# Performance work log

Hardware: AMD Instinct MI355X
Metric: run time of the kernel (lower is better)

Reference implementation:

```python
import jax, jax.numpy as jnp
import numpy as np

B = 4; D = 256; H = 8; L = 4; P = 4; DFF = 1024; DH = D // H
SHAPES = ((64, 64), (32, 32), (16, 16), (8, 8))
LEN = sum(h * w for h, w in SHAPES)  # 5440


def setup_inputs() -> dict:
    key = jax.random.key(0)
    ks = jax.random.split(key, 12)
    s = 0.02
    ss = jnp.array(SHAPES, jnp.int32)
    lsi = jnp.array(np.concatenate([[0], np.cumsum([h * w for h, w in SHAPES])[:-1]]), jnp.int32)
    return dict(
        src=jax.random.normal(ks[0], (B, LEN, D), jnp.float32),
        reference_points=jax.random.uniform(ks[1], (B, LEN, L, 2), jnp.float32),
        spatial_shapes=ss,
        level_start_index=lsi,
        padding_mask=jnp.zeros((B, LEN), bool),
        pos=jax.random.normal(ks[2], (B, LEN, D), jnp.float32),
        W_value=s * jax.random.normal(ks[3], (D, D), jnp.float32), b_value=jnp.zeros(D, jnp.float32),
        W_off=s * jax.random.normal(ks[4], (D, H * L * P * 2), jnp.float32), b_off=jnp.zeros(H * L * P * 2, jnp.float32),
        W_attn=s * jax.random.normal(ks[5], (D, H * L * P), jnp.float32), b_attn=jnp.zeros(H * L * P, jnp.float32),
        W_out=s * jax.random.normal(ks[6], (D, D), jnp.float32), b_out=jnp.zeros(D, jnp.float32),
        ln1_g=jnp.ones(D, jnp.float32), ln1_b=jnp.zeros(D, jnp.float32),
        W1=s * jax.random.normal(ks[7], (D, DFF), jnp.float32), b1=jnp.zeros(DFF, jnp.float32),
        W2=s * jax.random.normal(ks[8], (DFF, D), jnp.float32), b2=jnp.zeros(D, jnp.float32),
        ln2_g=jnp.ones(D, jnp.float32), ln2_b=jnp.zeros(D, jnp.float32),
    )


def layer_norm(x, g, b, eps=1e-5):
    m = jnp.mean(x, -1, keepdims=True)
    v = jnp.var(x, -1, keepdims=True)
    return (x - m) * jax.lax.rsqrt(v + eps) * g + b


def ms_deform_attn(query, src, reference_points, spatial_shapes, level_start_index, padding_mask,
                   W_value, b_value, W_off, b_off, W_attn, b_attn, W_out, b_out):
    Bq, Lq, C = query.shape
    Lin = src.shape[1]
    value = src @ W_value + b_value
    value = jnp.where(padding_mask[..., None], jnp.zeros((), value.dtype), value)
    value = value.reshape(Bq, Lin, H, DH).transpose(0, 2, 1, 3)  # [B,H,Lin,d]

    off = (query @ W_off + b_off).reshape(Bq, Lq, H, L, P, 2)
    attn = (query @ W_attn + b_attn).reshape(Bq, Lq, H, L * P)
    attn = jax.nn.softmax(attn, axis=-1).reshape(Bq, Lq, H, L, P)

    # offset normalizer is (W_l, H_l)
    norm = jnp.stack([spatial_shapes[:, 1], spatial_shapes[:, 0]], -1).astype(query.dtype)  # [L,2]
    loc = reference_points[:, :, None, :, None, :] + off / norm[None, None, None, :, None, :]  # [B,Lq,H,L,P,2]

    Hl = spatial_shapes[:, 0][None, None, None, :, None]  # [1,1,1,L,1]
    Wl = spatial_shapes[:, 1][None, None, None, :, None]
    start = level_start_index[None, None, None, :, None]
    # grid_sample align_corners=False: pixel = loc * size - 0.5
    px = loc[..., 0] * Wl.astype(query.dtype) - 0.5  # [B,Lq,H,L,P]
    py = loc[..., 1] * Hl.astype(query.dtype) - 0.5
    x0 = jnp.floor(px); y0 = jnp.floor(py)
    fx = px - x0; fy = py - y0
    x0i = x0.astype(jnp.int32); y0i = y0.astype(jnp.int32)

    out = jnp.zeros((Bq, Lq, H, DH), query.dtype)
    corners = ((0, 0, (1 - fx) * (1 - fy)), (1, 0, fx * (1 - fy)), (0, 1, (1 - fx) * fy), (1, 1, fx * fy))
    for dx, dy, cw in corners:
        xi = x0i + dx
        yi = y0i + dy
        valid = (xi >= 0) & (xi < Wl) & (yi >= 0) & (yi < Hl)  # zeros padding
        flat = start + jnp.clip(yi, 0, Hl - 1) * Wl + jnp.clip(xi, 0, Wl - 1)  # [B,Lq,H,L,P]
        w = attn * cw * valid.astype(query.dtype)  # [B,Lq,H,L,P]
        idx = flat.transpose(0, 2, 1, 3, 4).reshape(Bq, H, Lq * L * P)  # [B,H,N]
        g = jnp.take_along_axis(value, idx[..., None], axis=2)  # [B,H,N,d]
        g = g.reshape(Bq, H, Lq, L, P, DH)
        out = out + jnp.einsum('bqhlp,bhqlpd->bqhd', w, g)

    out = out.reshape(Bq, Lq, C)
    return out @ W_out + b_out


def reference(src, reference_points, spatial_shapes, level_start_index, padding_mask, pos,
              W_value, b_value, W_off, b_off, W_attn, b_attn, W_out, b_out,
              ln1_g, ln1_b, W1, b1, W2, b2, ln2_g, ln2_b):
    q = src + pos
    src2 = ms_deform_attn(q, src, reference_points, spatial_shapes, level_start_index, padding_mask,
                          W_value, b_value, W_off, b_off, W_attn, b_attn, W_out, b_out)
    x = layer_norm(src + src2, ln1_g, ln1_b)  # dropout is identity at eval
    ff = jax.nn.relu(x @ W1 + b1) @ W2 + b2
    return layer_norm(x + ff, ln2_g, ln2_b)
```

## Files before the change

### kernel.cpp

```cpp
#include <hip/hip_runtime.h>
#include <hip/hip_fp16.h>

constexpr int NB   = 4;
constexpr int SLEN = 5440;
constexpr long NTOK = (long)NB * SLEN;
constexpr int DD   = 256;
constexpr int NH   = 8;
constexpr int DHD  = 32;
constexpr int NL   = 4;
constexpr int NP   = 4;
constexpr int DFF  = 1024;

typedef __attribute__((ext_vector_type(8))) short short8;
typedef __attribute__((ext_vector_type(8))) unsigned short ushort8;
typedef __attribute__((ext_vector_type(4))) float f32x4;

static __device__ __forceinline__ unsigned short f2bf(float x) {
  union { float f; unsigned int u; } v; v.f = x;
  unsigned int r = v.u + 0x7fffu + ((v.u >> 16) & 1u);
  return (unsigned short)(r >> 16);
}
static __device__ __forceinline__ float bf2f(unsigned short u) {
  union { unsigned int i; float f; } v; v.i = ((unsigned int)u) << 16; return v.f;
}
static __device__ __forceinline__ unsigned int pack2bf(float lo, float hi) {
  return (unsigned int)f2bf(lo) | ((unsigned int)f2bf(hi) << 16);
}
static __device__ __forceinline__ unsigned int pack2h_dup(float a) {
  const unsigned int h = (unsigned int)__half_as_ushort(__float2half(a));
  return h | (h << 16);
}
static __device__ __forceinline__ __half2 u2h2(unsigned int u) {
  union { unsigned int i; __half2 h; } c; c.i = u; return c.h;
}

static __device__ __forceinline__ long fragpos(int k, int n, int KT) {
  const int kt = k >> 5, i = k & 7;
  const int lane = ((k >> 3) & 3) * 16 + (n & 15);
  const int nt = n >> 4;
  return (((long)(nt * KT + kt) * 64 + lane) * 8 + i);
}

__global__ __launch_bounds__(256) void k_prep_all(const float* __restrict__ W1,
                                                  const float* __restrict__ W2,
                                                  const float* __restrict__ Wv,
                                                  const float* __restrict__ Woff,
                                                  const float* __restrict__ Wattn,
                                                  const float* __restrict__ Wo,
                                                  unsigned short* __restrict__ W1f,
                                                  unsigned short* __restrict__ W2f,
                                                  unsigned short* __restrict__ Wvf,
                                                  unsigned short* __restrict__ Wqf,
                                                  unsigned short* __restrict__ Wof) {
  const int g = blockIdx.x * 256 + threadIdx.x;
  if (g < 262144) {
    const int k = g >> 10, n = g & 1023;
    W1f[fragpos(k, n, 8)] = f2bf(W1[g]);
  } else if (g < 524288) {
    const int g2 = g - 262144;
    const int k = g2 >> 8, n = g2 & 255;
    W2f[fragpos(k, n, 32)] = f2bf(W2[g2]);
  } else if (g < 589824) {
    const int g2 = g - 524288;
    const int k = g2 >> 8, n = g2 & 255;
    Wvf[fragpos(k, n, 8)] = f2bf(Wv[g2]);
  } else if (g < 688128) {
    const int g2 = g - 589824;
    const int k = g2 / 384, n = g2 % 384;
    const float w = (n < 256) ? Woff[k * 256 + n] : Wattn[k * 128 + (n - 256)];
    Wqf[fragpos(k, n, 8)] = f2bf(w);
  } else if (g < 753664) {
    const int g2 = g - 688128;
    const int k = g2 >> 8, n = g2 & 255;
    Wof[fragpos(k, n, 8)] = f2bf(Wo[g2]);
  }
}

__global__ __launch_bounds__(256) void k_vq2(const float* __restrict__ src,
                                             const float* __restrict__ pos,
                                             const unsigned short* __restrict__ Wvf,
                                             const float* __restrict__ bv,
                                             const unsigned short* __restrict__ Wqf,
                                             const float* __restrict__ boff,
                                             const float* __restrict__ battn,
                                             unsigned short* __restrict__ valh,
                                             unsigned short* __restrict__ offbf,
                                             float* __restrict__ attn) {
  __shared__ unsigned short Xs[32 * 256];
  const int t = threadIdx.x;
  const int w = t >> 6, lane = t & 63;
  const int lr = lane & 15, lgrp = lane >> 4;
  const long row0 = (long)blockIdx.x * 32;
  const int r = t >> 3;
  const int c0 = (t & 7) * 32;

  {
    const float* sp = &src[(row0 + r) * DD + c0];
#pragma unroll
    for (int j = 0; j < 4; ++j) {
      const float4 a = *reinterpret_cast<const float4*>(&sp[j * 8 + 0]);
      const float4 b = *reinterpret_cast<const float4*>(&sp[j * 8 + 4]);
      short8 pk;
      pk[0] = (short)f2bf(a.x); pk[1] = (short)f2bf(a.y);
      pk[2] = (short)f2bf(a.z); pk[3] = (short)f2bf(a.w);
      pk[4] = (short)f2bf(b.x); pk[5] = (short)f2bf(b.y);
      pk[6] = (short)f2bf(b.z); pk[7] = (short)f2bf(b.w);
      int byte = r * 512 + (c0 + j * 8) * 2;
      byte ^= (r & 7) << 4;
      *reinterpret_cast<short8*>(reinterpret_cast<char*>(Xs) + byte) = pk;
    }
  }
  __syncthreads();

  short8 af[2][8];
#pragma unroll
  for (int mt = 0; mt < 2; ++mt)
#pragma unroll
    for (int kt = 0; kt < 8; ++kt) {
      const int row = mt * 16 + lr;
      int byte = row * 512 + kt * 64 + lgrp * 16;
      byte ^= (row & 7) << 4;
      af[mt][kt] = *reinterpret_cast<const short8*>(reinterpret_cast<const char*>(Xs) + byte);
    }

  {
    f32x4 acc[2][4];
#pragma unroll
    for (int mt = 0; mt < 2; ++mt)
#pragma unroll
      for (int n = 0; n < 4; ++n) acc[mt][n] = (f32x4){0.f, 0.f, 0.f, 0.f};
#pragma unroll
    for (int n = 0; n < 4; ++n) {
      const int nt = w * 4 + n;
#pragma unroll
      for (int kt = 0; kt < 8; ++kt) {
        const short8 bf_ = *reinterpret_cast<const short8*>(&Wvf[((nt * 8 + kt) * 64 + lane) * 8]);
#pragma unroll
        for (int mt = 0; mt < 2; ++mt)
          acc[mt][n] = __builtin_amdgcn_mfma_f32_16x16x32_bf16(af[mt][kt], bf_, acc[mt][n], 0, 0, 0);
      }
    }
#pragma unroll
    for (int n = 0; n < 4; ++n) {
      const int col = w * 64 + n * 16 + lr;
      const float bb = bv[col];
#pragma unroll
      for (int mt = 0; mt < 2; ++mt)
#pragma unroll
        for (int j = 0; j < 4; ++j) {
          const int row = mt * 16 + lgrp * 4 + j;
          valh[(row0 + row) * DD + col] =
              __half_as_ushort(__float2half(acc[mt][n][j] + bb));
        }
    }
  }
  __syncthreads();

  {
    const float* pp = &pos[(row0 + r) * DD + c0];
#pragma unroll
    for (int j = 0; j < 4; ++j) {
      const float4 c = *reinterpret_cast<const float4*>(&pp[j * 8 + 0]);
      const float4 d = *reinterpret_cast<const float4*>(&pp[j * 8 + 4]);
      int byte = r * 512 + (c0 + j * 8) * 2;
      byte ^= (r & 7) << 4;
      short8 pk = *reinterpret_cast<const short8*>(reinterpret_cast<const char*>(Xs) + byte);
      pk[0] = (short)f2bf(bf2f((unsigned short)pk[0]) + c.x);
      pk[1] = (short)f2bf(bf2f((unsigned short)pk[1]) + c.y);
      pk[2] = (short)f2bf(bf2f((unsigned short)pk[2]) + c.z);
      pk[3] = (short)f2bf(bf2f((unsigned short)pk[3]) + c.w);
      pk[4] = (short)f2bf(bf2f((unsigned short)pk[4]) + d.x);
      pk[5] = (short)f2bf(bf2f((unsigned short)pk[5]) + d.y);
      pk[6] = (short)f2bf(bf2f((unsigned short)pk[6]) + d.z);
      pk[7] = (short)f2bf(bf2f((unsigned short)pk[7]) + d.w);
      *reinterpret_cast<short8*>(reinterpret_cast<char*>(Xs) + byte) = pk;
    }
  }
  __syncthreads();

#pragma unroll
  for (int mt = 0; mt < 2; ++mt)
#pragma unroll
    for (int kt = 0; kt < 8; ++kt) {
      const int row = mt * 16 + lr;
      int byte = row * 512 + kt * 64 + lgrp * 16;
      byte ^= (row & 7) << 4;
      af[mt][kt] = *reinterpret_cast<const short8*>(reinterpret_cast<const char*>(Xs) + byte);
    }

  {
    f32x4 acc[2][6];
#pragma unroll
    for (int mt = 0; mt < 2; ++mt)
#pragma unroll
      for (int i = 0; i < 6; ++i) acc[mt][i] = (f32x4){0.f, 0.f, 0.f, 0.f};
#pragma unroll
    for (int i = 0; i < 6; ++i) {
      const int ntg = w * 6 + i;
#pragma unroll
      for (int kt = 0; kt < 8; ++kt) {
        const short8 bf_ = *reinterpret_cast<const short8*>(&Wqf[((ntg * 8 + kt) * 64 + lane) * 8]);
#pragma unroll
        for (int mt = 0; mt < 2; ++mt)
          acc[mt][i] = __builtin_amdgcn_mfma_f32_16x16x32_bf16(af[mt][kt], bf_, acc[mt][i], 0, 0, 0);
      }
    }
#pragma unroll
    for (int i = 0; i < 6; ++i) {
      const int ntg = w * 6 + i;
      if (ntg < 16) {
        const int col = ntg * 16 + lr;
        const float bb = boff[col];
#pragma unroll
        for (int mt = 0; mt < 2; ++mt)
#pragma unroll
          for (int j = 0; j < 4; ++j) {
            const int row = mt * 16 + lgrp * 4 + j;
            offbf[(row0 + row) * 256 + col] = f2bf(acc[mt][i][j] + bb);
          }
      } else {
        const int na = ntg - 16;
        const float bb = battn[na * 16 + lr];
#pragma unroll
        for (int mt = 0; mt < 2; ++mt)
#pragma unroll
          for (int j = 0; j < 4; ++j) {
            const int row = mt * 16 + lgrp * 4 + j;
            const float v = acc[mt][i][j] + bb;
            float m = v;
#pragma unroll
            for (int d_ = 1; d_ <= 8; d_ <<= 1) m = fmaxf(m, __shfl_xor(m, d_, 16));
            const float e = __expf(v - m);
            float s = e;
#pragma unroll
            for (int d_ = 1; d_ <= 8; d_ <<= 1) s += __shfl_xor(s, d_, 16);
            attn[(row0 + row) * 128 + na * 16 + lr] = e / s;
          }
      }
    }
  }
}

__global__ __launch_bounds__(256) void k_sample6(const unsigned short* __restrict__ valh,
                                                 const unsigned short* __restrict__ offbf,
                                                 const float* __restrict__ attn,
                                                 const float* __restrict__ refp,
                                                 unsigned short* __restrict__ src2bf) {
  __shared__ int4  sIdx[4][2][8][16];
  __shared__ uint4 sWgt[4][2][8][16];
  const int t = threadIdx.x;
  const int w = t >> 6, lane = t & 63;
  const int tok = lane >> 5, hg = (lane >> 2) & 7, li = lane & 3;
  const int B = blockIdx.x;
  const int bimg = (B & 7) >> 1;
  const int ii = ((B >> 3) << 1) + (B & 1);
  const long n = (long)bimg * SLEN + ii * 8 + w * 2 + tok;
  const long bOff = (long)bimg * SLEN;

  const int   WlA[4] = {64, 32, 16, 8};
  const float rWA[4] = {1.f / 64.f, 1.f / 32.f, 1.f / 16.f, 1.f / 8.f};
  const int   stA[4] = {0, 4096, 5120, 5376};

#pragma unroll
  for (int q = 0; q < 4; ++q) {
    const int pt = q * 4 + li;
    const int Wi = WlA[q];
    const float Wf = (float)Wi, rW = rWA[q];
    const float rx = refp[(n * 4 + q) * 2 + 0];
    const float ry = refp[(n * 4 + q) * 2 + 1];
    const float aw = attn[n * 128 + hg * 16 + pt];
    const int oi = ((hg * 4 + q) * 4 + li) * 2;
    const unsigned int opk = *reinterpret_cast<const unsigned int*>(&offbf[n * 256 + oi]);
    const float ox = bf2f((unsigned short)(opk & 0xffff));
    const float oy = bf2f((unsigned short)(opk >> 16));
    const float px = (rx + ox * rW) * Wf - 0.5f;
    const float py = (ry + oy * rW) * Wf - 0.5f;
    const float x0f = floorf(px), y0f = floorf(py);
    const float fx = px - x0f, fy = py - y0f;
    const int x0 = (int)x0f, y0 = (int)y0f;
    int   ic[4];
    float wc[4];
#pragma unroll
    for (int c = 0; c < 4; ++c) {
      const int dx = c & 1, dy = c >> 1;
      const int xi = x0 + dx, yi = y0 + dy;
      const float cw = (dx ? fx : 1.f - fx) * (dy ? fy : 1.f - fy);
      const bool valid = (xi >= 0) && (xi < Wi) && (yi >= 0) && (yi < Wi);
      const int xc = min(max(xi, 0), Wi - 1);
      const int yc = min(max(yi, 0), Wi - 1);
      const long flat = stA[q] + yc * Wi + xc;
      ic[c] = (int)((bOff + flat) * DD + hg * DHD);
      wc[c] = aw * cw * (valid ? 1.f : 0.f);
    }
    const int slot = pt ^ hg;
    sIdx[w][tok][hg][slot] = make_int4(ic[0], ic[1], ic[2], ic[3]);
    sWgt[w][tok][hg][slot] = make_uint4(pack2h_dup(wc[0]), pack2h_dup(wc[1]),
                                        pack2h_dup(wc[2]), pack2h_dup(wc[3]));
  }
  __syncthreads();

  __half2 acc[4];
#pragma unroll
  for (int d = 0; d < 4; ++d) acc[d] = __float2half2_rn(0.f);
#pragma unroll 4
  for (int pt = 0; pt < 16; ++pt) {
    const int slot = pt ^ hg;
    const int4  ia = sIdx[w][tok][hg][slot];
    const uint4 wp = sWgt[w][tok][hg][slot];
    const uint4 u0 = *reinterpret_cast<const uint4*>(&valh[(long)ia.x + li * 8]);
    const uint4 u1 = *reinterpret_cast<const uint4*>(&valh[(long)ia.y + li * 8]);
    const uint4 u2 = *reinterpret_cast<const uint4*>(&valh[(long)ia.z + li * 8]);
    const uint4 u3 = *reinterpret_cast<const uint4*>(&valh[(long)ia.w + li * 8]);
    const __half2 w0 = u2h2(wp.x), w1 = u2h2(wp.y), w2 = u2h2(wp.z), w3 = u2h2(wp.w);
    acc[0] = __hfma2(u2h2(u0.x), w0, acc[0]);
    acc[1] = __hfma2(u2h2(u0.y), w0, acc[1]);
    acc[2] = __hfma2(u2h2(u0.z), w0, acc[2]);
    acc[3] = __hfma2(u2h2(u0.w), w0, acc[3]);
    acc[0] = __hfma2(u2h2(u1.x), w1, acc[0]);
    acc[1] = __hfma2(u2h2(u1.y), w1, acc[1]);
    acc[2] = __hfma2(u2h2(u1.z), w1, acc[2]);
    acc[3] = __hfma2(u2h2(u1.w), w1, acc[3]);
    acc[0] = __hfma2(u2h2(u2.x), w2, acc[0]);
    acc[1] = __hfma2(u2h2(u2.y), w2, acc[1]);
    acc[2] = __hfma2(u2h2(u2.z), w2, acc[2]);
    acc[3] = __hfma2(u2h2(u2.w), w2, acc[3]);
    acc[0] = __hfma2(u2h2(u3.x), w3, acc[0]);
    acc[1] = __hfma2(u2h2(u3.y), w3, acc[1]);
    acc[2] = __hfma2(u2h2(u3.z), w3, acc[2]);
    acc[3] = __hfma2(u2h2(u3.w), w3, acc[3]);
  }
  ushort8 o;
#pragma unroll
  for (int d = 0; d < 4; ++d) {
    o[2 * d]     = f2bf(__half2float(__low2half(acc[d])));
    o[2 * d + 1] = f2bf(__half2float(__high2half(acc[d])));
  }
  *reinterpret_cast<ushort8*>(&src2bf[n * DD + hg * DHD + li * 8]) = o;
}

__global__ __launch_bounds__(256) void k_outproj_mfma(const unsigned short* __restrict__ src2bf,
                                                      const unsigned short* __restrict__ Wof,
                                                      const float* __restrict__ bo,
                                                      const float* __restrict__ src,
                                                      const float* __restrict__ g1,
                                                      const float* __restrict__ b1g,
                                                      unsigned short* __restrict__ xbf) {
  __shared__ float rsum[32][4];
  __shared__ float rssq[32][4];
  const int t = threadIdx.x;
  const int w = t >> 6, lane = t & 63;
  const int lr = lane & 15, lgrp = lane >> 4;
  const long row0 = (long)blockIdx.x * 32;

  short8 af[2][8];
#pragma unroll
  for (int mt = 0; mt < 2; ++mt)
#pragma unroll
    for (int kt = 0; kt < 8; ++kt)
      af[mt][kt] = *reinterpret_cast<const short8*>(
          &src2bf[(row0 + mt * 16 + lr) * DD + kt * 32 + lgrp * 8]);

  f32x4 acc[2][4];
#pragma unroll
  for (int mt = 0; mt < 2; ++mt)
#pragma unroll
    for (int n = 0; n < 4; ++n) acc[mt][n] = (f32x4){0.f, 0.f, 0.f, 0.f};
#pragma unroll
  for (int n = 0; n < 4; ++n) {
    const int nt = w * 4 + n;
#pragma unroll
    for (int kt = 0; kt < 8; ++kt) {
      const short8 bf_ = *reinterpret_cast<const short8*>(&Wof[((nt * 8 + kt) * 64 + lane) * 8]);
#pragma unroll
      for (int mt = 0; mt < 2; ++mt)
        acc[mt][n] = __builtin_amdgcn_mfma_f32_16x16x32_bf16(af[mt][kt], bf_, acc[mt][n], 0, 0, 0);
    }
  }
  float bc[4], gc[4], bgc[4];
#pragma unroll
  for (int n = 0; n < 4; ++n) {
    const int col = w * 64 + n * 16 + lr;
    bc[n] = bo[col]; gc[n] = g1[col]; bgc[n] = b1g[col];
  }
  float vals[2][4][4];
#pragma unroll
  for (int mt = 0; mt < 2; ++mt)
#pragma unroll
    for (int j = 0; j < 4; ++j) {
      const int row = mt * 16 + lgrp * 4 + j;
      float s = 0.f, ss = 0.f;
#pragma unroll
      for (int n = 0; n < 4; ++n) {
        const int col = w * 64 + n * 16 + lr;
        const float v = acc[mt][n][j] + bc[n] + src[(row0 + row) * DD + col];
        vals[mt][n][j] = v;
        s += v; ss += v * v;
      }
#pragma unroll
      for (int m = 1; m <= 8; m <<= 1) { s += __shfl_xor(s, m, 64); ss += __shfl_xor(ss, m, 64); }
      if (lr == 0) { rsum[row][w] = s; rssq[row][w] = ss; }
    }
  __syncthreads();
#pragma unroll
  for (int mt = 0; mt < 2; ++mt)
#pragma unroll
    for (int j = 0; j < 4; ++j) {
      const int row = mt * 16 + lgrp * 4 + j;
      const float s  = rsum[row][0] + rsum[row][1] + rsum[row][2] + rsum[row][3];
      const float ss = rssq[row][0] + rssq[row][1] + rssq[row][2] + rssq[row][3];
      const float mean = s * (1.f / 256.f);
      const float inv  = rsqrtf(ss * (1.f / 256.f) - mean * mean + 1e-5f);
#pragma unroll
      for (int n = 0; n < 4; ++n) {
        const int col = w * 64 + n * 16 + lr;
        xbf[(row0 + row) * DD + col] = f2bf((vals[mt][n][j] - mean) * inv * gc[n] + bgc[n]);
      }
    }
}

__global__ __launch_bounds__(256) void k_ffn1e(const unsigned short* __restrict__ xbf,
                                               const unsigned short* __restrict__ W1f,
                                               const float* __restrict__ b1v,
                                               unsigned short* __restrict__ hfrag) {
  const int t = threadIdx.x;
  const int w = t >> 6, lane = t & 63;
  const int lr = lane & 15, lgrp = lane >> 4;
  const long row0 = (long)blockIdx.x * 64;
  const int hg = blockIdx.y;

  f32x4 acc[4][4];
#pragma unroll
  for (int mm = 0; mm < 4; ++mm)
#pragma unroll
    for (int n = 0; n < 4; ++n) acc[mm][n] = (f32x4){0.f, 0.f, 0.f, 0.f};

#pragma unroll
  for (int kt = 0; kt < 8; ++kt) {
    short8 bx[4];
#pragma unroll
    for (int n = 0; n < 4; ++n)
      bx[n] = *reinterpret_cast<const short8*>(
          &xbf[(row0 + n * 16 + lr) * DD + kt * 32 + lgrp * 8]);
#pragma unroll
    for (int mm = 0; mm < 4; ++mm) {
      const int ntg = hg * 16 + w * 4 + mm;
      const short8 aw1 = *reinterpret_cast<const short8*>(&W1f[((ntg * 8 + kt) * 64 + lane) * 8]);
#pragma unroll
      for (int n = 0; n < 4; ++n)
        acc[mm][n] = __builtin_amdgcn_mfma_f32_16x16x32_bf16(aw1, bx[n], acc[mm][n], 0, 0, 0);
    }
  }

#pragma unroll
  for (int mm = 0; mm < 4; ++mm) {
    const int ht = hg * 16 + w * 4 + mm;
    const float4 bq = *reinterpret_cast<const float4*>(&b1v[ht * 16 + lgrp * 4]);
#pragma unroll
    for (int n = 0; n < 4; ++n) {
      const long tt = (long)blockIdx.x * 4 + n;
      const long tbase = (tt * 64 + ht) * 256;
      int2 pk;
      pk.x = (int)pack2bf(fmaxf(acc[mm][n][0] + bq.x, 0.f),
                          fmaxf(acc[mm][n][1] + bq.y, 0.f));
      pk.y = (int)pack2bf(fmaxf(acc[mm][n][2] + bq.z, 0.f),
                          fmaxf(acc[mm][n][3] + bq.w, 0.f));
      *reinterpret_cast<int2*>(&hfrag[tbase + lane * 4]) = pk;
    }
  }
}

__global__ __launch_bounds__(256) void k_ffn2t(const unsigned short* __restrict__ hfrag,
                                               const unsigned short* __restrict__ W2f,
                                               const float* __restrict__ b2v_,
                                               const unsigned short* __restrict__ xbf,
                                               const float* __restrict__ g2,
                                               const float* __restrict__ b2g,
                                               float* __restrict__ outp) {
  __shared__ float rsum[32][4];
  __shared__ float rssq[32][4];
  const int t = threadIdx.x;
  const int w = t >> 6, lane = t & 63;
  const int lr = lane & 15, lgrp = lane >> 4;
  const long row0 = (long)blockIdx.x * 32;

  f32x4 acc[2][4];
#pragma unroll
  for (int mt = 0; mt < 2; ++mt)
#pragma unroll
    for (int n = 0; n < 4; ++n) acc[mt][n] = (f32x4){0.f, 0.f, 0.f, 0.f};

#pragma unroll 4
  for (int kt = 0; kt < 32; ++kt) {
    short8 ha[2];
#pragma unroll
    for (int mt = 0; mt < 2; ++mt) {
      const long tt = (row0 >> 4) + mt;
      const long tb = (tt * 64 + kt * 2 + (lgrp >> 1)) * 256;
      const unsigned short* tp = &hfrag[tb + (lgrp & 1) * 128 + lr * 4];
      union { short8 s8; struct { int2 lo, hi; } p; } u;
      u.p.lo = *reinterpret_cast<const int2*>(tp);
      u.p.hi = *reinterpret_cast<const int2*>(tp + 64);
      ha[mt] = u.s8;
    }
#pragma unroll
    for (int n = 0; n < 4; ++n) {
      const int nt = w * 4 + n;
      const short8 bf_ = *reinterpret_cast<const short8*>(&W2f[((nt * 32 + kt) * 64 + lane) * 8]);
#pragma unroll
      for (int mt = 0; mt < 2; ++mt)
        acc[mt][n] = __builtin_amdgcn_mfma_f32_16x16x32_bf16(ha[mt], bf_, acc[mt][n], 0, 0, 0);
    }
  }

  float b2c[4], g2c[4], bgc[4];
#pragma unroll
  for (int n = 0; n < 4; ++n) {
    const int col = w * 64 + n * 16 + lr;
    b2c[n] = b2v_[col]; g2c[n] = g2[col]; bgc[n] = b2g[col];
  }
  float vals[2][4][4];
#pragma unroll
  for (int mt = 0; mt < 2; ++mt)
#pragma unroll
    for (int j = 0; j < 4; ++j) {
      const int row = mt * 16 + lgrp * 4 + j;
      float s = 0.f, ss = 0.f;
#pragma unroll
      for (int n = 0; n < 4; ++n) {
        const int col = w * 64 + n * 16 + lr;
        const float v = acc[mt][n][j] + b2c[n] + bf2f(xbf[(row0 + row) * DD + col]);
        vals[mt][n][j] = v;
        s += v; ss += v * v;
      }
#pragma unroll
      for (int m = 1; m <= 8; m <<= 1) { s += __shfl_xor(s, m, 64); ss += __shfl_xor(ss, m, 64); }
      if (lr == 0) { rsum[row][w] = s; rssq[row][w] = ss; }
    }
  __syncthreads();
#pragma unroll
  for (int mt = 0; mt < 2; ++mt)
#pragma unroll
    for (int j = 0; j < 4; ++j) {
      const int row = mt * 16 + lgrp * 4 + j;
      const float s  = rsum[row][0] + rsum[row][1] + rsum[row][2] + rsum[row][3];
      const float ss = rssq[row][0] + rssq[row][1] + rssq[row][2] + rssq[row][3];
      const float mean = s * (1.f / 256.f);
      const float inv  = rsqrtf(ss * (1.f / 256.f) - mean * mean + 1e-5f);
#pragma unroll
      for (int n = 0; n < 4; ++n) {
        const int col = w * 64 + n * 16 + lr;
        outp[(row0 + row) * DD + col] = (vals[mt][n][j] - mean) * inv * g2c[n] + bgc[n];
      }
    }
}

extern "C" void kernel_launch(void* const* d_in, const int* in_sizes, int n_in,
                              void* d_out, int out_size, void* d_ws, size_t ws_size,
                              hipStream_t stream) {
  const float* src  = (const float*)d_in[0];
  const float* refp = (const float*)d_in[1];
  const float* pos  = (const float*)d_in[5];
  const float* Wv   = (const float*)d_in[6];
  const float* bv   = (const float*)d_in[7];
  const float* Woff = (const float*)d_in[8];
  const float* boff = (const float*)d_in[9];
  const float* Wat  = (const float*)d_in[10];
  const float* bat  = (const float*)d_in[11];
  const float* Wo   = (const float*)d_in[12];
  const float* bo   = (const float*)d_in[13];
  const float* g1   = (const float*)d_in[14];
  const float* b1g  = (const float*)d_in[15];
  const float* W1   = (const float*)d_in[16];
  const float* b1f  = (const float*)d_in[17];
  const float* W2   = (const float*)d_in[18];
  const float* b2f  = (const float*)d_in[19];
  const float* g2   = (const float*)d_in[20];
  const float* b2g  = (const float*)d_in[21];
  float* out = (float*)d_out;

  unsigned short* valh   = (unsigned short*)d_ws;
  unsigned short* offbf  = valh + NTOK * 256;
  float*          attn   = (float*)(offbf + NTOK * 256);
  unsigned short* src2bf = (unsigned short*)(attn + NTOK * 128);
  unsigned short* xbf    = src2bf + NTOK * 256;
  unsigned short* W1f = xbf + NTOK * 256;
  unsigned short* W2f = W1f + 262144;
  unsigned short* Wvf = W2f + 262144;
  unsigned short* Wqf = Wvf + 65536;
  unsigned short* Wof = Wqf + 98304;
  unsigned short* frag_end = Wof + 65536;
  const size_t used  = (size_t)((char*)frag_end - (char*)d_ws);
  const size_t hneed = (size_t)NTOK * 1024 * 2;
  unsigned short* hfrag = (used + hneed <= ws_size) ? frag_end
                                                    : (unsigned short*)d_ws;

  hipLaunchKernelGGL(k_prep_all, dim3(2944), dim3(256), 0, stream,
                     W1, W2, Wv, Woff, Wat, Wo, W1f, W2f, Wvf, Wqf, Wof);
  hipLaunchKernelGGL(k_vq2, dim3((int)(NTOK / 32)), dim3(256), 0, stream,
                     src, pos, Wvf, bv, Wqf, boff, bat, valh, offbf, attn);
  hipLaunchKernelGGL(k_sample6, dim3((int)(NTOK / 8)), dim3(256), 0, stream,
                     valh, offbf, attn, refp, src2bf);
  hipLaunchKernelGGL(k_outproj_mfma, dim3((int)(NTOK / 32)), dim3(256), 0, stream,
                     src2bf, Wof, bo, src, g1, b1g, xbf);
  hipLaunchKernelGGL(k_ffn1e, dim3((int)(NTOK / 64), 4), dim3(256), 0, stream,
                     xbf, W1f, b1f, hfrag);
  hipLaunchKernelGGL(k_ffn2t, dim3((int)(NTOK / 32)), dim3(256), 0, stream,
                     hfrag, W2f, b2f, xbf, g2, b2g, out);
}
```

Before: 160.0 us.

## Fuse out-projection, LayerNorm, FFN1 and FFN2 into one LDS-resident tail kernel

Merges the out-projection+LN1, FFN first layer and FFN second layer+LN2 kernels into a single kernel per 32-token block. The normalized activations and the 1024-wide hidden layer live in XOR-swizzled shared memory (80 KB) instead of round-tripping through global memory. This removes two launches and the global write and read of the hidden activations. The costs are lower occupancy from the large LDS allocation and W1 being re-read per 32-row block instead of per 64-row block.

```diff
diff --git a/kernel.cpp b/kernel.cpp
--- a/kernel.cpp
+++ b/kernel.cpp
@@ -338,15 +338,25 @@
   *reinterpret_cast<ushort8*>(&src2bf[n * DD + hg * DHD + li * 8]) = o;
 }
 
-__global__ __launch_bounds__(256) void k_outproj_mfma(const unsigned short* __restrict__ src2bf,
-                                                      const unsigned short* __restrict__ Wof,
-                                                      const float* __restrict__ bo,
-                                                      const float* __restrict__ src,
-                                                      const float* __restrict__ g1,
-                                                      const float* __restrict__ b1g,
-                                                      unsigned short* __restrict__ xbf) {
-  __shared__ float rsum[32][4];
-  __shared__ float rssq[32][4];
+__global__ __launch_bounds__(256) void k_tail(const unsigned short* __restrict__ src2bf,
+                                              const unsigned short* __restrict__ Wof,
+                                              const float* __restrict__ bo,
+                                              const float* __restrict__ src,
+                                              const float* __restrict__ g1,
+                                              const float* __restrict__ b1g,
+                                              const unsigned short* __restrict__ W1f,
+                                              const float* __restrict__ b1v,
+                                              const unsigned short* __restrict__ W2f,
+                                              const float* __restrict__ b2v_,
+                                              const float* __restrict__ g2,
+                                              const float* __restrict__ b2g,
+                                              float* __restrict__ outp) {
+  __shared__ char smem[81920];
+  unsigned short* Xls = (unsigned short*)smem;
+  unsigned short* Hls = (unsigned short*)(smem + 16384);
+  float* rsum = (float*)(smem + 16384);
+  float* rssq = rsum + 128;
+
   const int t = threadIdx.x;
   const int w = t >> 6, lane = t & 63;
   const int lr = lane & 15, lgrp = lane >> 4;
@@ -376,13 +386,132 @@
         acc[mt][n] = __builtin_amdgcn_mfma_f32_16x16x32_bf16(af[mt][kt], bf_, acc[mt][n], 0, 0, 0);
     }
   }
-  float bc[4], gc[4], bgc[4];
+  {
+    float bc[4], gc[4], bgc[4];
+#pragma unroll
+    for (int n = 0; n < 4; ++n) {
+      const int col = w * 64 + n * 16 + lr;
+      bc[n] = bo[col]; gc[n] = g1[col]; bgc[n] = b1g[col];
+    }
+    float vals[2][4][4];
+#pragma unroll
+    for (int mt = 0; mt < 2; ++mt)
+#pragma unroll
+      for (int j = 0; j < 4; ++j) {
+        const int row = mt * 16 + lgrp * 4 + j;
+        float s = 0.f, ss = 0.f;
+#pragma unroll
+        for (int n = 0; n < 4; ++n) {
+          const int col = w * 64 + n * 16 + lr;
+          const float v = acc[mt][n][j] + bc[n] + src[(row0 + row) * DD + col];
+          vals[mt][n][j] = v;
+          s += v; ss += v * v;
+        }
+#pragma unroll
+        for (int m = 1; m <= 8; m <<= 1) { s += __shfl_xor(s, m, 64); ss += __shfl_xor(ss, m, 64); }
+        if (lr == 0) { rsum[row * 4 + w] = s; rssq[row * 4 + w] = ss; }
+      }
+    __syncthreads();
+#pragma unroll
+    for (int mt = 0; mt < 2; ++mt)
+#pragma unroll
+      for (int j = 0; j < 4; ++j) {
+        const int row = mt * 16 + lgrp * 4 + j;
+        const float s  = rsum[row * 4 + 0] + rsum[row * 4 + 1] + rsum[row * 4 + 2] + rsum[row * 4 + 3];
+        const float ss = rssq[row * 4 + 0] + rssq[row * 4 + 1] + rssq[row * 4 + 2] + rssq[row * 4 + 3];
+        const float mean = s * (1.f / 256.f);
+        const float inv  = rsqrtf(ss * (1.f / 256.f) - mean * mean + 1e-5f);
+#pragma unroll
+        for (int n = 0; n < 4; ++n) {
+          const int col = w * 64 + n * 16 + lr;
+          const float xv = (vals[mt][n][j] - mean) * inv * gc[n] + bgc[n];
+          int byte = row * 512 + col * 2;
+          byte ^= (row & 7) << 4;
+          *reinterpret_cast<unsigned short*>(reinterpret_cast<char*>(Xls) + byte) = f2bf(xv);
+        }
+      }
+  }
+  __syncthreads();
+
+#pragma unroll
+  for (int hp = 0; hp < 2; ++hp) {
+    f32x4 a2[8][2];
+#pragma unroll
+    for (int mm = 0; mm < 8; ++mm)
+#pragma unroll
+      for (int n = 0; n < 2; ++n) a2[mm][n] = (f32x4){0.f, 0.f, 0.f, 0.f};
+#pragma unroll
+    for (int kt = 0; kt < 8; ++kt) {
+      short8 bx[2];
+#pragma unroll
+      for (int n = 0; n < 2; ++n) {
+        const int row = n * 16 + lr;
+        int byte = row * 512 + kt * 64 + lgrp * 16;
+        byte ^= (row & 7) << 4;
+        bx[n] = *reinterpret_cast<const short8*>(reinterpret_cast<const char*>(Xls) + byte);
+      }
+#pragma unroll
+      for (int mm = 0; mm < 8; ++mm) {
+        const int ntg = w * 16 + hp * 8 + mm;
+        const short8 aw1 = *reinterpret_cast<const short8*>(&W1f[((ntg * 8 + kt) * 64 + lane) * 8]);
+#pragma unroll
+        for (int n = 0; n < 2; ++n)
+          a2[mm][n] = __builtin_amdgcn_mfma_f32_16x16x32_bf16(aw1, bx[n], a2[mm][n], 0, 0, 0);
+      }
+    }
+#pragma unroll
+    for (int mm = 0; mm < 8; ++mm) {
+      const int ht = w * 16 + hp * 8 + mm;
+      const float4 bq = *reinterpret_cast<const float4*>(&b1v[ht * 16 + lgrp * 4]);
+#pragma unroll
+      for (int n = 0; n < 2; ++n) {
+        const int tok = n * 16 + lr;
+        int2 pk;
+        pk.x = (int)pack2bf(fmaxf(a2[mm][n][0] + bq.x, 0.f),
+                            fmaxf(a2[mm][n][1] + bq.y, 0.f));
+        pk.y = (int)pack2bf(fmaxf(a2[mm][n][2] + bq.z, 0.f),
+                            fmaxf(a2[mm][n][3] + bq.w, 0.f));
+        int byte = tok * 2048 + (ht * 16 + lgrp * 4) * 2;
+        byte ^= (tok & 7) << 4;
+        *reinterpret_cast<int2*>(reinterpret_cast<char*>(Hls) + byte) = pk;
+      }
+    }
+  }
+  __syncthreads();
+
+  f32x4 c2[2][4];
+#pragma unroll
+  for (int mt = 0; mt < 2; ++mt)
+#pragma unroll
+    for (int n = 0; n < 4; ++n) c2[mt][n] = (f32x4){0.f, 0.f, 0.f, 0.f};
+#pragma unroll 4
+  for (int kt = 0; kt < 32; ++kt) {
+    short8 ha[2];
+#pragma unroll
+    for (int mt = 0; mt < 2; ++mt) {
+      const int row = mt * 16 + lr;
+      int byte = row * 2048 + kt * 64 + lgrp * 16;
+      byte ^= (row & 7) << 4;
+      ha[mt] = *reinterpret_cast<const short8*>(reinterpret_cast<const char*>(Hls) + byte);
+    }
+#pragma unroll
+    for (int n = 0; n < 4; ++n) {
+      const int nt = w * 4 + n;
+      const short8 bf_ = *reinterpret_cast<const short8*>(&W2f[((nt * 32 + kt) * 64 + lane) * 8]);
+#pragma unroll
+      for (int mt = 0; mt < 2; ++mt)
+        c2[mt][n] = __builtin_amdgcn_mfma_f32_16x16x32_bf16(ha[mt], bf_, c2[mt][n], 0, 0, 0);
+    }
+  }
+
+  float b2c[4], g2c[4], bgc2[4];
 #pragma unroll
   for (int n = 0; n < 4; ++n) {
     const int col = w * 64 + n * 16 + lr;
-    bc[n] = bo[col]; gc[n] = g1[col]; bgc[n] = b1g[col];
-  }
-  float vals[2][4][4];
+    b2c[n] = b2v_[col]; g2c[n] = g2[col]; bgc2[n] = b2g[col];
+  }
+  float vals2[2][4][4];
+  float sP[2][4], ssP[2][4];
 #pragma unroll
   for (int mt = 0; mt < 2; ++mt)
 #pragma unroll
@@ -392,13 +521,17 @@
 #pragma unroll
       for (int n = 0; n < 4; ++n) {
         const int col = w * 64 + n * 16 + lr;
-        const float v = acc[mt][n][j] + bc[n] + src[(row0 + row) * DD + col];
-        vals[mt][n][j] = v;
+        int byte = row * 512 + col * 2;
+        byte ^= (row & 7) << 4;
+        const float xv = bf2f(*reinterpret_cast<const unsigned short*>(
+            reinterpret_cast<const char*>(Xls) + byte));
+        const float v = c2[mt][n][j] + b2c[n] + xv;
+        vals2[mt][n][j] = v;
         s += v; ss += v * v;
       }
 #pragma unroll
       for (int m = 1; m <= 8; m <<= 1) { s += __shfl_xor(s, m, 64); ss += __shfl_xor(ss, m, 64); }
-      if (lr == 0) { rsum[row][w] = s; rssq[row][w] = ss; }
+      sP[mt][j] = s; ssP[mt][j] = ss;
     }
   __syncthreads();
 #pragma unroll
@@ -406,150 +539,22 @@
 #pragma unroll
     for (int j = 0; j < 4; ++j) {
       const int row = mt * 16 + lgrp * 4 + j;
-      const float s  = rsum[row][0] + rsum[row][1] + rsum[row][2] + rsum[row][3];
-      const float ss = rssq[row][0] + rssq[row][1] + rssq[row][2] + rssq[row][3];
+      if (lr == 0) { rsum[row * 4 + w] = sP[mt][j]; rssq[row * 4 + w] = ssP[mt][j]; }
+    }
+  __syncthreads();
+#pragma unroll
+  for (int mt = 0; mt < 2; ++mt)
+#pragma unroll
+    for (int j = 0; j < 4; ++j) {
+      const int row = mt * 16 + lgrp * 4 + j;
+      const float s  = rsum[row * 4 + 0] + rsum[row * 4 + 1] + rsum[row * 4 + 2] + rsum[row * 4 + 3];
+      const float ss = rssq[row * 4 + 0] + rssq[row * 4 + 1] + rssq[row * 4 + 2] + rssq[row * 4 + 3];
       const float mean = s * (1.f / 256.f);
       const float inv  = rsqrtf(ss * (1.f / 256.f) - mean * mean + 1e-5f);
 #pragma unroll
       for (int n = 0; n < 4; ++n) {
         const int col = w * 64 + n * 16 + lr;
-        xbf[(row0 + row) * DD + col] = f2bf((vals[mt][n][j] - mean) * inv * gc[n] + bgc[n]);
-      }
-    }
-}
-
-__global__ __launch_bounds__(256) void k_ffn1e(const unsigned short* __restrict__ xbf,
-                                               const unsigned short* __restrict__ W1f,
-                                               const float* __restrict__ b1v,
-                                               unsigned short* __restrict__ hfrag) {
-  const int t = threadIdx.x;
-  const int w = t >> 6, lane = t & 63;
-  const int lr = lane & 15, lgrp = lane >> 4;
-  const long row0 = (long)blockIdx.x * 64;
-  const int hg = blockIdx.y;
-
-  f32x4 acc[4][4];
-#pragma unroll
-  for (int mm = 0; mm < 4; ++mm)
-#pragma unroll
-    for (int n = 0; n < 4; ++n) acc[mm][n] = (f32x4){0.f, 0.f, 0.f, 0.f};
-
-#pragma unroll
-  for (int kt = 0; kt < 8; ++kt) {
-    short8 bx[4];
-#pragma unroll
-    for (int n = 0; n < 4; ++n)
-      bx[n] = *reinterpret_cast<const short8*>(
-          &xbf[(row0 + n * 16 + lr) * DD + kt * 32 + lgrp * 8]);
-#pragma unroll
-    for (int mm = 0; mm < 4; ++mm) {
-      const int ntg = hg * 16 + w * 4 + mm;
-      const short8 aw1 = *reinterpret_cast<const short8*>(&W1f[((ntg * 8 + kt) * 64 + lane) * 8]);
-#pragma unroll
-      for (int n = 0; n < 4; ++n)
-        acc[mm][n] = __builtin_amdgcn_mfma_f32_16x16x32_bf16(aw1, bx[n], acc[mm][n], 0, 0, 0);
-    }
-  }
-
-#pragma unroll
-  for (int mm = 0; mm < 4; ++mm) {
-    const int ht = hg * 16 + w * 4 + mm;
-    const float4 bq = *reinterpret_cast<const float4*>(&b1v[ht * 16 + lgrp * 4]);
-#pragma unroll
-    for (int n = 0; n < 4; ++n) {
-      const long tt = (long)blockIdx.x * 4 + n;
-      const long tbase = (tt * 64 + ht) * 256;
-      int2 pk;
-      pk.x = (int)pack2bf(fmaxf(acc[mm][n][0] + bq.x, 0.f),
-                          fmaxf(acc[mm][n][1] + bq.y, 0.f));
-      pk.y = (int)pack2bf(fmaxf(acc[mm][n][2] + bq.z, 0.f),
-                          fmaxf(acc[mm][n][3] + bq.w, 0.f));
-      *reinterpret_cast<int2*>(&hfrag[tbase + lane * 4]) = pk;
-    }
-  }
-}
-
-__global__ __launch_bounds__(256) void k_ffn2t(const unsigned short* __restrict__ hfrag,
-                                               const unsigned short* __restrict__ W2f,
-                                               const float* __restrict__ b2v_,
-                                               const unsigned short* __restrict__ xbf,
-                                               const float* __restrict__ g2,
-                                               const float* __restrict__ b2g,
-                                               float* __restrict__ outp) {
-  __shared__ float rsum[32][4];
-  __shared__ float rssq[32][4];
-  const int t = threadIdx.x;
-  const int w = t >> 6, lane = t & 63;
-  const int lr = lane & 15, lgrp = lane >> 4;
-  const long row0 = (long)blockIdx.x * 32;
-
-  f32x4 acc[2][4];
-#pragma unroll
-  for (int mt = 0; mt < 2; ++mt)
-#pragma unroll
-    for (int n = 0; n < 4; ++n) acc[mt][n] = (f32x4){0.f, 0.f, 0.f, 0.f};
-
-#pragma unroll 4
-  for (int kt = 0; kt < 32; ++kt) {
-    short8 ha[2];
-#pragma unroll
-    for (int mt = 0; mt < 2; ++mt) {
-      const long tt = (row0 >> 4) + mt;
-      const long tb = (tt * 64 + kt * 2 + (lgrp >> 1)) * 256;
-      const unsigned short* tp = &hfrag[tb + (lgrp & 1) * 128 + lr * 4];
-      union { short8 s8; struct { int2 lo, hi; } p; } u;
-      u.p.lo = *reinterpret_cast<const int2*>(tp);
-      u.p.hi = *reinterpret_cast<const int2*>(tp + 64);
-      ha[mt] = u.s8;
-    }
-#pragma unroll
-    for (int n = 0; n < 4; ++n) {
-      const int nt = w * 4 + n;
-      const short8 bf_ = *reinterpret_cast<const short8*>(&W2f[((nt * 32 + kt) * 64 + lane) * 8]);
-#pragma unroll
-      for (int mt = 0; mt < 2; ++mt)
-        acc[mt][n] = __builtin_amdgcn_mfma_f32_16x16x32_bf16(ha[mt], bf_, acc[mt][n], 0, 0, 0);
-    }
-  }
-
-  float b2c[4], g2c[4], bgc[4];
-#pragma unroll
-  for (int n = 0; n < 4; ++n) {
-    const int col = w * 64 + n * 16 + lr;
-    b2c[n] = b2v_[col]; g2c[n] = g2[col]; bgc[n] = b2g[col];
-  }
-  float vals[2][4][4];
-#pragma unroll
-  for (int mt = 0; mt < 2; ++mt)
-#pragma unroll
-    for (int j = 0; j < 4; ++j) {
-      const int row = mt * 16 + lgrp * 4 + j;
-      float s = 0.f, ss = 0.f;
-#pragma unroll
-      for (int n = 0; n < 4; ++n) {
-        const int col = w * 64 + n * 16 + lr;
-        const float v = acc[mt][n][j] + b2c[n] + bf2f(xbf[(row0 + row) * DD + col]);
-        vals[mt][n][j] = v;
-        s += v; ss += v * v;
-      }
-#pragma unroll
-      for (int m = 1; m <= 8; m <<= 1) { s += __shfl_xor(s, m, 64); ss += __shfl_xor(ss, m, 64); }
-      if (lr == 0) { rsum[row][w] = s; rssq[row][w] = ss; }
-    }
-  __syncthreads();
-#pragma unroll
-  for (int mt = 0; mt < 2; ++mt)
-#pragma unroll
-    for (int j = 0; j < 4; ++j) {
-      const int row = mt * 16 + lgrp * 4 + j;
-      const float s  = rsum[row][0] + rsum[row][1] + rsum[row][2] + rsum[row][3];
-      const float ss = rssq[row][0] + rssq[row][1] + rssq[row][2] + rssq[row][3];
-      const float mean = s * (1.f / 256.f);
-      const float inv  = rsqrtf(ss * (1.f / 256.f) - mean * mean + 1e-5f);
-#pragma unroll
-      for (int n = 0; n < 4; ++n) {
-        const int col = w * 64 + n * 16 + lr;
-        outp[(row0 + row) * DD + col] = (vals[mt][n][j] - mean) * inv * g2c[n] + bgc[n];
+        outp[(row0 + row) * DD + col] = (vals2[mt][n][j] - mean) * inv * g2c[n] + bgc2[n];
       }
     }
 }
@@ -582,17 +587,11 @@
   unsigned short* offbf  = valh + NTOK * 256;
   float*          attn   = (float*)(offbf + NTOK * 256);
   unsigned short* src2bf = (unsigned short*)(attn + NTOK * 128);
-  unsigned short* xbf    = src2bf + NTOK * 256;
-  unsigned short* W1f = xbf + NTOK * 256;
+  unsigned short* W1f = src2bf + NTOK * 256;
   unsigned short* W2f = W1f + 262144;
   unsigned short* Wvf = W2f + 262144;
   unsigned short* Wqf = Wvf + 65536;
   unsigned short* Wof = Wqf + 98304;
-  unsigned short* frag_end = Wof + 65536;
-  const size_t used  = (size_t)((char*)frag_end - (char*)d_ws);
-  const size_t hneed = (size_t)NTOK * 1024 * 2;
-  unsigned short* hfrag = (used + hneed <= ws_size) ? frag_end
-                                                    : (unsigned short*)d_ws;
 
   hipLaunchKernelGGL(k_prep_all, dim3(2944), dim3(256), 0, stream,
                      W1, W2, Wv, Woff, Wat, Wo, W1f, W2f, Wvf, Wqf, Wof);
@@ -600,10 +599,6 @@
                      src, pos, Wvf, bv, Wqf, boff, bat, valh, offbf, attn);
   hipLaunchKernelGGL(k_sample6, dim3((int)(NTOK / 8)), dim3(256), 0, stream,
                      valh, offbf, attn, refp, src2bf);
-  hipLaunchKernelGGL(k_outproj_mfma, dim3((int)(NTOK / 32)), dim3(256), 0, stream,
-                     src2bf, Wof, bo, src, g1, b1g, xbf);
-  hipLaunchKernelGGL(k_ffn1e, dim3((int)(NTOK / 64), 4), dim3(256), 0, stream,
-                     xbf, W1f, b1f, hfrag);
-  hipLaunchKernelGGL(k_ffn2t, dim3((int)(NTOK / 32)), dim3(256), 0, stream,
-                     hfrag, W2f, b2f, xbf, g2, b2g, out);
-}
+  hipLaunchKernelGGL(k_tail, dim3((int)(NTOK / 32)), dim3(256), 0, stream,
+                     src2bf, Wof, bo, src, g1, b1g, W1f, b1f, W2f, b2f, g2, b2g, out);
+}
```

Result: slower. 195.4 us (+22.2%).
